# Kernel optimization log

Measured on AMD Instinct MI355X. Metric: run time of the kernel, lower is better.

The kernel has to match this reference:

```python
import jax, jax.numpy as jnp
import numpy as np

N, E, H, L, G = 50000, 500000, 128, 4, 1000
EPS = 1e-7      # GENConv message eps
LN_EPS = 1e-5   # torch LayerNorm default


def setup_inputs() -> dict:
    key = jax.random.key(0)
    ks = jax.random.split(key, 24)
    d = {}
    d["x"] = jax.random.normal(ks[0], (N, 9), jnp.float32)
    d["edge_index"] = jax.random.randint(ks[1], (2, E), 0, N, jnp.int32)
    d["edge_attr"] = jax.random.normal(ks[2], (E, 3), jnp.float32)
    d["batch"] = jnp.sort(jax.random.randint(ks[3], (N,), 0, G, jnp.int32))
    s9, s3, sh, s2h = 1/np.sqrt(9), 1/np.sqrt(3), 1/np.sqrt(H), 1/np.sqrt(2*H)
    u = lambda k, shp, s: jax.random.uniform(k, shp, jnp.float32, -s, s)
    d["enc_node_W"] = u(ks[4], (9, H), s9)
    d["enc_node_b"] = u(ks[5], (H,), s9)
    d["enc_edge_W"] = u(ks[6], (3, H), s3)
    d["enc_edge_b"] = u(ks[7], (H,), s3)
    d["ln_g"] = jnp.ones((L, H), jnp.float32)   # DeepGCNLayer pre-norm affine
    d["ln_b"] = jnp.zeros((L, H), jnp.float32)
    d["W1"] = u(ks[8], (L, H, 2*H), sh)          # GENConv MLP layer 1
    d["b1"] = u(ks[9], (L, 2*H), sh)
    d["mlp_ln_g"] = jnp.ones((L, 2*H), jnp.float32)
    d["mlp_ln_b"] = jnp.zeros((L, 2*H), jnp.float32)
    d["W2"] = u(ks[10], (L, 2*H, H), s2h)        # GENConv MLP layer 2
    d["b2"] = u(ks[11], (L, H), s2h)
    d["t"] = jnp.ones((L,), jnp.float32)         # learnable softmax temperature, init 1.0
    return d


def layernorm(x, g, b):
    mu = x.mean(-1, keepdims=True)
    var = ((x - mu) ** 2).mean(-1, keepdims=True)
    return (x - mu) / jnp.sqrt(var + LN_EPS) * g + b


def genconv(h, src, dst, ea, t, W1, b1, lg, lb, W2, b2):
    # message: relu(x_j + edge_attr) + eps   -> [E, H]
    msg = jax.nn.relu(h[src] + ea) + EPS
    # softmax aggregation over incoming edges, per channel
    logits = t * msg
    m = jax.ops.segment_max(logits, dst, num_segments=N)
    num = jnp.exp(logits - m[dst])
    den = jax.ops.segment_sum(num, dst, num_segments=N)
    alpha = num / den[dst]
    agg = jax.ops.segment_sum(msg * alpha, dst, num_segments=N)
    out = agg + h  # root residual inside GENConv
    z = jax.nn.relu(layernorm(out @ W1 + b1, lg, lb))
    return z @ W2 + b2


def reference(x, edge_index, edge_attr, batch, enc_node_W, enc_node_b,
              enc_edge_W, enc_edge_b, ln_g, ln_b, W1, b1, mlp_ln_g, mlp_ln_b,
              W2, b2, t):
    src, dst = edge_index[0], edge_index[1]
    h = x @ enc_node_W + enc_node_b            # node encoder  [N, H]
    ea = edge_attr @ enc_edge_W + enc_edge_b   # edge encoder  [E, H]
    # layer 0: conv only (DeeperGCN forward uses layers[0].conv directly)
    h = genconv(h, src, dst, ea, t[0], W1[0], b1[0], mlp_ln_g[0], mlp_ln_b[0], W2[0], b2[0])
    # layers 1..L-1: res+ block: x + conv(relu(LN(x))); dropout is identity (eval)
    for i in range(1, L):
        z = jax.nn.relu(layernorm(h, ln_g[i], ln_b[i]))
        h = h + genconv(z, src, dst, ea, t[i], W1[i], b1[i], mlp_ln_g[i], mlp_ln_b[i], W2[i], b2[i])
    h = jax.nn.relu(layernorm(h, ln_g[0], ln_b[0]))  # reuses layer-0 norm
    # global mean pool over graphs
    counts = jax.ops.segment_sum(jnp.ones((N,), h.dtype), batch, num_segments=G)
    sums = jax.ops.segment_sum(h, batch, num_segments=G)
    return sums / jnp.maximum(counts, 1.0)[:, None]
```

## Files before the change

### kernel.cpp

```cpp
#include <hip/hip_runtime.h>

#define NN 50000
#define NE 500000
#define HD 128
#define HD2 256
#define NL 4
#define NG 1000

constexpr float MSG_EPS = 1e-7f;
constexpr float LNEPS   = 1e-5f;

typedef float  f32x4  __attribute__((ext_vector_type(4)));
typedef __bf16 bf16x8 __attribute__((ext_vector_type(8)));

__device__ __forceinline__ unsigned short f2b(float f) {
    unsigned int u = __float_as_uint(f);
    unsigned int r = u + 0x7FFFu + ((u >> 16) & 1u);
    return (unsigned short)(r >> 16);
}
__device__ __forceinline__ float b2f(unsigned short h) {
    return __uint_as_float(((unsigned int)h) << 16);
}

__global__ void k_encode_nodes(const float* __restrict__ x, const float* __restrict__ W,
                               const float* __restrict__ b, unsigned short* __restrict__ zb) {
    int n = blockIdx.x;
    int c = threadIdx.x;
    float xr[9];
#pragma unroll
    for (int k = 0; k < 9; k++) xr[k] = x[n * 9 + k];
    float acc = b[c];
#pragma unroll
    for (int k = 0; k < 9; k++) acc = fmaf(xr[k], W[k * HD + c], acc);
    zb[n * HD + c] = f2b(acc);
}

__global__ void k_prep(const float* __restrict__ W1, const float* __restrict__ W2,
                       unsigned short* __restrict__ W1T, unsigned short* __restrict__ W2T) {
    int idx = blockIdx.x * 256 + threadIdx.x;
    {
        int k = idx & 127, n = (idx >> 7) & 255, l = idx >> 15;
        W1T[idx] = f2b(W1[(l * 128 + k) * 256 + n]);
    }
    {
        int k = idx & 255, n = (idx >> 8) & 127, l = idx >> 15;
        W2T[idx] = f2b(W2[(l * 256 + k) * 128 + n]);
    }
}

__global__ void k_hist(const int* __restrict__ dst, int* __restrict__ counts) {
    int e = blockIdx.x * blockDim.x + threadIdx.x;
    if (e < NE) atomicAdd(&counts[dst[e]], 1);
}

#define SCAN_B 512
__global__ void k_scan1(const int* __restrict__ counts, int* __restrict__ incl,
                        int* __restrict__ bsum) {
    __shared__ int s[SCAN_B];
    int i = blockIdx.x * SCAN_B + threadIdx.x;
    int v = (i < NN) ? counts[i] : 0;
    s[threadIdx.x] = v;
    __syncthreads();
    for (int off = 1; off < SCAN_B; off <<= 1) {
        int t = (threadIdx.x >= off) ? s[threadIdx.x - off] : 0;
        __syncthreads();
        s[threadIdx.x] += t;
        __syncthreads();
    }
    if (i < NN) incl[i] = s[threadIdx.x];
    if (threadIdx.x == SCAN_B - 1) bsum[blockIdx.x] = s[threadIdx.x];
}

__global__ void k_scan2(const int* __restrict__ bsum, int* __restrict__ boff, int nb) {
    __shared__ int s[128];
    int v = (threadIdx.x < nb) ? bsum[threadIdx.x] : 0;
    s[threadIdx.x] = v;
    __syncthreads();
    for (int off = 1; off < 128; off <<= 1) {
        int t = (threadIdx.x >= off) ? s[threadIdx.x - off] : 0;
        __syncthreads();
        s[threadIdx.x] += t;
        __syncthreads();
    }
    if (threadIdx.x < nb) boff[threadIdx.x] = s[threadIdx.x] - v;
}

__global__ void k_scan3(const int* __restrict__ incl, const int* __restrict__ boff,
                        int* __restrict__ row_start) {
    int i = blockIdx.x * SCAN_B + threadIdx.x;
    if (i < NN) row_start[i + 1] = incl[i] + boff[blockIdx.x];
    if (i == 0) row_start[0] = 0;
}

__global__ void k_scatter(const int* __restrict__ src, const int* __restrict__ dst,
                          const float* __restrict__ eattr, const int* __restrict__ row_start,
                          int* __restrict__ cursor, float4* __restrict__ aperm) {
    int e = blockIdx.x * blockDim.x + threadIdx.x;
    if (e >= NE) return;
    int d = dst[e];
    int p = row_start[d] + atomicAdd(&cursor[d], 1);
    float4 v;
    v.x = eattr[e * 3 + 0];
    v.y = eattr[e * 3 + 1];
    v.z = eattr[e * 3 + 2];
    v.w = __int_as_float(src[e]);
    aperm[p] = v;
}

__global__ __launch_bounds__(256) void k_aggregate(const unsigned short* __restrict__ zb,
                                                   const float4* __restrict__ aperm,
                                                   const int* __restrict__ row_start,
                                                   const float* __restrict__ We,
                                                   const float* __restrict__ be,
                                                   const float* __restrict__ t, int layer,
                                                   unsigned int* __restrict__ outb) {
    int w = threadIdx.x >> 6, lane = threadIdx.x & 63;
    int n = blockIdx.x * 4 + w;
    if (n >= NN) return;
    int c = lane * 2;
    float2 w0 = *(const float2*)&We[c];
    float2 w1 = *(const float2*)&We[HD + c];
    float2 w2 = *(const float2*)&We[2 * HD + c];
    float2 bb = *(const float2*)&be[c];
    float tv = t[layer];
    int s0 = row_start[n], s1 = row_start[n + 1];
    float num0 = 0.f, num1 = 0.f, wm0 = 0.f, wm1 = 0.f;
    const unsigned int* z32 = (const unsigned int*)zb;
    int p = s0;
    for (; p + 2 <= s1; p += 2) {
        float4 a0 = aperm[p];
        float4 a1 = aperm[p + 1];
        int sj0 = __float_as_int(a0.w);
        int sj1 = __float_as_int(a1.w);
        unsigned int za = z32[sj0 * 64 + lane];
        unsigned int zc = z32[sj1 * 64 + lane];
        float zax = b2f((unsigned short)za), zay = b2f((unsigned short)(za >> 16));
        float zcx = b2f((unsigned short)zc), zcy = b2f((unsigned short)(zc >> 16));
        float ea0x = fmaf(a0.x, w0.x, fmaf(a0.y, w1.x, fmaf(a0.z, w2.x, bb.x)));
        float ea0y = fmaf(a0.x, w0.y, fmaf(a0.y, w1.y, fmaf(a0.z, w2.y, bb.y)));
        float ea1x = fmaf(a1.x, w0.x, fmaf(a1.y, w1.x, fmaf(a1.z, w2.x, bb.x)));
        float ea1y = fmaf(a1.x, w0.y, fmaf(a1.y, w1.y, fmaf(a1.z, w2.y, bb.y)));
        float m0x = fmaxf(zax + ea0x, 0.f) + MSG_EPS;
        float m0y = fmaxf(zay + ea0y, 0.f) + MSG_EPS;
        float m1x = fmaxf(zcx + ea1x, 0.f) + MSG_EPS;
        float m1y = fmaxf(zcy + ea1y, 0.f) + MSG_EPS;
        float e0x = __expf(tv * m0x), e0y = __expf(tv * m0y);
        float e1x = __expf(tv * m1x), e1y = __expf(tv * m1y);
        num0 += e0x + e1x;
        num1 += e0y + e1y;
        wm0 = fmaf(m0x, e0x, fmaf(m1x, e1x, wm0));
        wm1 = fmaf(m0y, e0y, fmaf(m1y, e1y, wm1));
    }
    if (p < s1) {
        float4 a = aperm[p];
        int sj = __float_as_int(a.w);
        unsigned int za = z32[sj * 64 + lane];
        float zax = b2f((unsigned short)za), zay = b2f((unsigned short)(za >> 16));
        float eax = fmaf(a.x, w0.x, fmaf(a.y, w1.x, fmaf(a.z, w2.x, bb.x)));
        float eay = fmaf(a.x, w0.y, fmaf(a.y, w1.y, fmaf(a.z, w2.y, bb.y)));
        float mx = fmaxf(zax + eax, 0.f) + MSG_EPS;
        float my = fmaxf(zay + eay, 0.f) + MSG_EPS;
        float ex = __expf(tv * mx), ey = __expf(tv * my);
        num0 += ex;
        num1 += ey;
        wm0 = fmaf(mx, ex, wm0);
        wm1 = fmaf(my, ey, wm1);
    }
    unsigned int zn = z32[n * 64 + lane];
    float ox = ((s1 > s0) ? (wm0 / num0) : 0.f) + b2f((unsigned short)zn);
    float oy = ((s1 > s0) ? (wm1 / num1) : 0.f) + b2f((unsigned short)(zn >> 16));
    outb[n * 64 + lane] = (unsigned int)f2b(ox) | ((unsigned int)f2b(oy) << 16);
}

#define HS_LD 268

__global__ __launch_bounds__(64) void k_mlp(const unsigned short* __restrict__ outb,
                                            const unsigned short* __restrict__ W1T,
                                            const float* __restrict__ b1l,
                                            const float* __restrict__ lgl,
                                            const float* __restrict__ lbl,
                                            const unsigned short* __restrict__ W2T,
                                            const float* __restrict__ b2l,
                                            unsigned short* __restrict__ h,
                                            const float* __restrict__ gn,
                                            const float* __restrict__ bn,
                                            unsigned short* __restrict__ zb,
                                            int add_residual) {
    __shared__ __align__(16) unsigned short Hs[16 * HS_LD];

    int base = blockIdx.x * 16;
    int lane = threadIdx.x;
    int q = lane >> 4, i = lane & 15;

    f32x4 acc[16];
#pragma unroll
    for (int ct = 0; ct < 16; ct++) acc[ct] = (f32x4){0.f, 0.f, 0.f, 0.f};

#pragma unroll
    for (int ks = 0; ks < 4; ks++) {
        bf16x8 a = *(const bf16x8*)&outb[(size_t)(base + i) * HD + ks * 32 + q * 8];
#pragma unroll
        for (int ct = 0; ct < 16; ct++) {
            bf16x8 bfr = *(const bf16x8*)&W1T[(ct * 16 + i) * HD + ks * 32 + q * 8];
            acc[ct] = __builtin_amdgcn_mfma_f32_16x16x32_bf16(a, bfr, acc[ct], 0, 0, 0);
        }
    }

#pragma unroll
    for (int ct = 0; ct < 16; ct++) {
        float bb = b1l[ct * 16 + i];
#pragma unroll
        for (int r = 0; r < 4; r++) acc[ct][r] += bb;
    }

    {
        float s[4] = {0.f, 0.f, 0.f, 0.f}, sq[4] = {0.f, 0.f, 0.f, 0.f};
#pragma unroll
        for (int ct = 0; ct < 16; ct++)
#pragma unroll
            for (int r = 0; r < 4; r++) {
                s[r] += acc[ct][r];
                sq[r] = fmaf(acc[ct][r], acc[ct][r], sq[r]);
            }
#pragma unroll
        for (int m = 8; m >= 1; m >>= 1)
#pragma unroll
            for (int r = 0; r < 4; r++) {
                s[r] += __shfl_xor(s[r], m);
                sq[r] += __shfl_xor(sq[r], m);
            }
        float mu[4], inv[4];
#pragma unroll
        for (int r = 0; r < 4; r++) {
            mu[r] = s[r] * (1.f / 256.f);
            float var = sq[r] * (1.f / 256.f) - mu[r] * mu[r];
            inv[r] = rsqrtf(var + LNEPS);
        }
#pragma unroll
        for (int ct = 0; ct < 16; ct++) {
            float g = lgl[ct * 16 + i];
            float c = lbl[ct * 16 + i];
#pragma unroll
            for (int r = 0; r < 4; r++) {
                float v = fmaxf(fmaf((acc[ct][r] - mu[r]) * inv[r], g, c), 0.f);
                Hs[(q * 4 + r) * HS_LD + ct * 16 + i] = f2b(v);
            }
        }
    }

    f32x4 acc2[8];
#pragma unroll
    for (int ct = 0; ct < 8; ct++) acc2[ct] = (f32x4){0.f, 0.f, 0.f, 0.f};

#pragma unroll
    for (int ks = 0; ks < 8; ks++) {
        bf16x8 a = *(const bf16x8*)&Hs[i * HS_LD + ks * 32 + q * 8];
#pragma unroll
        for (int ct = 0; ct < 8; ct++) {
            bf16x8 bfr = *(const bf16x8*)&W2T[(ct * 16 + i) * HD2 + ks * 32 + q * 8];
            acc2[ct] = __builtin_amdgcn_mfma_f32_16x16x32_bf16(a, bfr, acc2[ct], 0, 0, 0);
        }
    }

    if (add_residual) {
#pragma unroll
        for (int ct = 0; ct < 8; ct++) {
            float bb = b2l[ct * 16 + i];
#pragma unroll
            for (int r = 0; r < 4; r++) {
                size_t idx = (size_t)(base + q * 4 + r) * HD + ct * 16 + i;
                acc2[ct][r] += bb + b2f(h[idx]);
            }
        }
    } else {
#pragma unroll
        for (int ct = 0; ct < 8; ct++) {
            float bb = b2l[ct * 16 + i];
#pragma unroll
            for (int r = 0; r < 4; r++) acc2[ct][r] += bb;
        }
    }
#pragma unroll
    for (int ct = 0; ct < 8; ct++)
#pragma unroll
        for (int r = 0; r < 4; r++) {
            size_t idx = (size_t)(base + q * 4 + r) * HD + ct * 16 + i;
            h[idx] = f2b(acc2[ct][r]);
        }

    {
        float s[4] = {0.f, 0.f, 0.f, 0.f}, sq[4] = {0.f, 0.f, 0.f, 0.f};
#pragma unroll
        for (int ct = 0; ct < 8; ct++)
#pragma unroll
            for (int r = 0; r < 4; r++) {
                s[r] += acc2[ct][r];
                sq[r] = fmaf(acc2[ct][r], acc2[ct][r], sq[r]);
            }
#pragma unroll
        for (int m = 8; m >= 1; m >>= 1)
#pragma unroll
            for (int r = 0; r < 4; r++) {
                s[r] += __shfl_xor(s[r], m);
                sq[r] += __shfl_xor(sq[r], m);
            }
        float mu[4], inv[4];
#pragma unroll
        for (int r = 0; r < 4; r++) {
            mu[r] = s[r] * (1.f / 128.f);
            float var = sq[r] * (1.f / 128.f) - mu[r] * mu[r];
            inv[r] = rsqrtf(var + LNEPS);
        }
#pragma unroll
        for (int ct = 0; ct < 8; ct++) {
            float g = gn[ct * 16 + i];
            float c = bn[ct * 16 + i];
#pragma unroll
            for (int r = 0; r < 4; r++) {
                float v = fmaxf(fmaf((acc2[ct][r] - mu[r]) * inv[r], g, c), 0.f);
                zb[(size_t)(base + q * 4 + r) * HD + ct * 16 + i] = f2b(v);
            }
        }
    }
}

__global__ void k_gbounds(const int* __restrict__ batch, int* __restrict__ gstart) {
    int g = blockIdx.x * blockDim.x + threadIdx.x;
    if (g > NG) return;
    int lo = 0, hi = NN;
    while (lo < hi) {
        int mid = (lo + hi) >> 1;
        if (batch[mid] < g) lo = mid + 1;
        else hi = mid;
    }
    gstart[g] = lo;
}

__global__ void k_pool(const unsigned short* __restrict__ zb, const int* __restrict__ gstart,
                       float* __restrict__ out) {
    int g = blockIdx.x;
    int c = threadIdx.x;
    int a = gstart[g], b = gstart[g + 1];
    float s0 = 0.f, s1 = 0.f;
    int n = a;
    for (; n + 2 <= b; n += 2) {
        s0 += b2f(zb[(size_t)n * HD + c]);
        s1 += b2f(zb[(size_t)(n + 1) * HD + c]);
    }
    if (n < b) s0 += b2f(zb[(size_t)n * HD + c]);
    out[g * HD + c] = (s0 + s1) / fmaxf((float)(b - a), 1.f);
}

extern "C" void kernel_launch(void* const* d_in, const int* in_sizes, int n_in, void* d_out,
                              int out_size, void* d_ws, size_t ws_size, hipStream_t stream) {
    const float* x     = (const float*)d_in[0];
    const int* ei      = (const int*)d_in[1];
    const float* eattr = (const float*)d_in[2];
    const int* batch   = (const int*)d_in[3];
    const float* encW  = (const float*)d_in[4];
    const float* encB  = (const float*)d_in[5];
    const float* eW    = (const float*)d_in[6];
    const float* eB    = (const float*)d_in[7];
    const float* ln_g  = (const float*)d_in[8];
    const float* ln_b  = (const float*)d_in[9];
    const float* W1    = (const float*)d_in[10];
    const float* b1    = (const float*)d_in[11];
    const float* mlg   = (const float*)d_in[12];
    const float* mlb   = (const float*)d_in[13];
    const float* W2    = (const float*)d_in[14];
    const float* b2    = (const float*)d_in[15];
    const float* t     = (const float*)d_in[16];
    const int* src = ei;
    const int* dst = ei + NE;

    char* w = (char*)d_ws;
    auto alloc = [&](size_t bytes) {
        char* p = w;
        w += (bytes + 255) & ~size_t(255);
        return p;
    };
    unsigned short* h    = (unsigned short*)alloc(sizeof(unsigned short) * NN * HD);
    unsigned short* zb   = (unsigned short*)alloc(sizeof(unsigned short) * NN * HD);
    unsigned int* outb   = (unsigned int*)alloc(sizeof(unsigned int) * NN * HD / 2);
    float4* aperm        = (float4*)alloc(sizeof(float4) * NE);
    int* row_start       = (int*)alloc(sizeof(int) * (NN + 1));
    int* counts          = (int*)alloc(sizeof(int) * NN);
    int* cursor          = (int*)alloc(sizeof(int) * NN);
    int* incl            = (int*)alloc(sizeof(int) * NN);
    int* bsum            = (int*)alloc(sizeof(int) * 128);
    int* boff            = (int*)alloc(sizeof(int) * 128);
    int* gstart          = (int*)alloc(sizeof(int) * (NG + 1));
    unsigned short* W1T  = (unsigned short*)alloc(sizeof(unsigned short) * NL * HD * HD2);
    unsigned short* W2T  = (unsigned short*)alloc(sizeof(unsigned short) * NL * HD2 * HD);

    hipMemsetAsync(counts, 0, sizeof(int) * NN, stream);
    hipMemsetAsync(cursor, 0, sizeof(int) * NN, stream);

    k_prep<<<512, 256, 0, stream>>>(W1, W2, W1T, W2T);
    k_encode_nodes<<<NN, HD, 0, stream>>>(x, encW, encB, zb);
    k_hist<<<(NE + 255) / 256, 256, 0, stream>>>(dst, counts);
    int nsb = (NN + SCAN_B - 1) / SCAN_B;
    k_scan1<<<nsb, SCAN_B, 0, stream>>>(counts, incl, bsum);
    k_scan2<<<1, 128, 0, stream>>>(bsum, boff, nsb);
    k_scan3<<<nsb, SCAN_B, 0, stream>>>(incl, boff, row_start);
    k_scatter<<<(NE + 255) / 256, 256, 0, stream>>>(src, dst, eattr, row_start, cursor, aperm);
    k_gbounds<<<(NG + 256) / 256, 256, 0, stream>>>(batch, gstart);

    for (int l = 0; l < NL; l++) {
        k_aggregate<<<(NN + 3) / 4, 256, 0, stream>>>(zb, aperm, row_start, eW, eB, t, l, outb);
        int ln_next = (l + 1) % NL;
        k_mlp<<<NN / 16, 64, 0, stream>>>(
            (const unsigned short*)outb, W1T + (size_t)l * HD * HD2, b1 + l * HD2,
            mlg + l * HD2, mlb + l * HD2, W2T + (size_t)l * HD2 * HD, b2 + l * HD, h,
            ln_g + ln_next * HD, ln_b + ln_next * HD, zb, l > 0);
    }
    k_pool<<<NG, HD, 0, stream>>>(zb, gstart, (float*)d_out);
}
```

Measured before the change: 586.1 us.

## Fuse edge aggregation and node MLP into one per-layer kernel

Merges the softmax aggregation kernel and the MFMA MLP kernel into a single kernel per layer. Each wave aggregates 16 nodes into LDS and then feeds that tile straight into the MLP, so the bf16 intermediate buffer never goes through global memory. Ping-pong z buffers are added to avoid read/write hazards across blocks. The edge loop is also unrolled by four to keep more gathers in flight. In exchange, each wave walks its 16 nodes one after another, so parallelism during the aggregation phase drops and per-block LDS use grows, which may reduce occupancy.

```diff
diff --git a/kernel.cpp b/kernel.cpp
--- a/kernel.cpp
+++ b/kernel.cpp
@@ -107,105 +107,91 @@
     aperm[p] = v;
 }
 
-__global__ __launch_bounds__(256) void k_aggregate(const unsigned short* __restrict__ zb,
-                                                   const float4* __restrict__ aperm,
-                                                   const int* __restrict__ row_start,
-                                                   const float* __restrict__ We,
-                                                   const float* __restrict__ be,
-                                                   const float* __restrict__ t, int layer,
-                                                   unsigned int* __restrict__ outb) {
+__device__ __forceinline__ void edge_acc(float4 a, unsigned int zz, float2 w0, float2 w1,
+                                         float2 w2, float2 bb, float tv, float& num0,
+                                         float& num1, float& wm0, float& wm1) {
+    float zx = b2f((unsigned short)zz), zy = b2f((unsigned short)(zz >> 16));
+    float eax = fmaf(a.x, w0.x, fmaf(a.y, w1.x, fmaf(a.z, w2.x, bb.x)));
+    float eay = fmaf(a.x, w0.y, fmaf(a.y, w1.y, fmaf(a.z, w2.y, bb.y)));
+    float mx = fmaxf(zx + eax, 0.f) + MSG_EPS;
+    float my = fmaxf(zy + eay, 0.f) + MSG_EPS;
+    float ex = __expf(tv * mx), ey = __expf(tv * my);
+    num0 += ex;
+    num1 += ey;
+    wm0 = fmaf(mx, ex, wm0);
+    wm1 = fmaf(my, ey, wm1);
+}
+
+#define AS_LD 136
+#define HS_LD 268
+
+__global__ __launch_bounds__(256) void k_layer(
+    const unsigned short* __restrict__ zbin, const float4* __restrict__ aperm,
+    const int* __restrict__ row_start, const float* __restrict__ We,
+    const float* __restrict__ be, const float* __restrict__ t, int layer,
+    const unsigned short* __restrict__ W1T, const float* __restrict__ b1l,
+    const float* __restrict__ lgl, const float* __restrict__ lbl,
+    const unsigned short* __restrict__ W2T, const float* __restrict__ b2l,
+    unsigned short* __restrict__ h, const float* __restrict__ gn,
+    const float* __restrict__ bn, unsigned short* __restrict__ zbout, int add_residual) {
+    __shared__ __align__(16) unsigned short lds[4 * (16 * AS_LD + 16 * HS_LD)];
+
     int w = threadIdx.x >> 6, lane = threadIdx.x & 63;
-    int n = blockIdx.x * 4 + w;
-    if (n >= NN) return;
-    int c = lane * 2;
-    float2 w0 = *(const float2*)&We[c];
-    float2 w1 = *(const float2*)&We[HD + c];
-    float2 w2 = *(const float2*)&We[2 * HD + c];
-    float2 bb = *(const float2*)&be[c];
-    float tv = t[layer];
-    int s0 = row_start[n], s1 = row_start[n + 1];
-    float num0 = 0.f, num1 = 0.f, wm0 = 0.f, wm1 = 0.f;
-    const unsigned int* z32 = (const unsigned int*)zb;
-    int p = s0;
-    for (; p + 2 <= s1; p += 2) {
-        float4 a0 = aperm[p];
-        float4 a1 = aperm[p + 1];
-        int sj0 = __float_as_int(a0.w);
-        int sj1 = __float_as_int(a1.w);
-        unsigned int za = z32[sj0 * 64 + lane];
-        unsigned int zc = z32[sj1 * 64 + lane];
-        float zax = b2f((unsigned short)za), zay = b2f((unsigned short)(za >> 16));
-        float zcx = b2f((unsigned short)zc), zcy = b2f((unsigned short)(zc >> 16));
-        float ea0x = fmaf(a0.x, w0.x, fmaf(a0.y, w1.x, fmaf(a0.z, w2.x, bb.x)));
-        float ea0y = fmaf(a0.x, w0.y, fmaf(a0.y, w1.y, fmaf(a0.z, w2.y, bb.y)));
-        float ea1x = fmaf(a1.x, w0.x, fmaf(a1.y, w1.x, fmaf(a1.z, w2.x, bb.x)));
-        float ea1y = fmaf(a1.x, w0.y, fmaf(a1.y, w1.y, fmaf(a1.z, w2.y, bb.y)));
-        float m0x = fmaxf(zax + ea0x, 0.f) + MSG_EPS;
-        float m0y = fmaxf(zay + ea0y, 0.f) + MSG_EPS;
-        float m1x = fmaxf(zcx + ea1x, 0.f) + MSG_EPS;
-        float m1y = fmaxf(zcy + ea1y, 0.f) + MSG_EPS;
-        float e0x = __expf(tv * m0x), e0y = __expf(tv * m0y);
-        float e1x = __expf(tv * m1x), e1y = __expf(tv * m1y);
-        num0 += e0x + e1x;
-        num1 += e0y + e1y;
-        wm0 = fmaf(m0x, e0x, fmaf(m1x, e1x, wm0));
-        wm1 = fmaf(m0y, e0y, fmaf(m1y, e1y, wm1));
-    }
-    if (p < s1) {
-        float4 a = aperm[p];
-        int sj = __float_as_int(a.w);
-        unsigned int za = z32[sj * 64 + lane];
-        float zax = b2f((unsigned short)za), zay = b2f((unsigned short)(za >> 16));
-        float eax = fmaf(a.x, w0.x, fmaf(a.y, w1.x, fmaf(a.z, w2.x, bb.x)));
-        float eay = fmaf(a.x, w0.y, fmaf(a.y, w1.y, fmaf(a.z, w2.y, bb.y)));
-        float mx = fmaxf(zax + eax, 0.f) + MSG_EPS;
-        float my = fmaxf(zay + eay, 0.f) + MSG_EPS;
-        float ex = __expf(tv * mx), ey = __expf(tv * my);
-        num0 += ex;
-        num1 += ey;
-        wm0 = fmaf(mx, ex, wm0);
-        wm1 = fmaf(my, ey, wm1);
-    }
-    unsigned int zn = z32[n * 64 + lane];
-    float ox = ((s1 > s0) ? (wm0 / num0) : 0.f) + b2f((unsigned short)zn);
-    float oy = ((s1 > s0) ? (wm1 / num1) : 0.f) + b2f((unsigned short)(zn >> 16));
-    outb[n * 64 + lane] = (unsigned int)f2b(ox) | ((unsigned int)f2b(oy) << 16);
-}
-
-#define HS_LD 268
-
-__global__ __launch_bounds__(64) void k_mlp(const unsigned short* __restrict__ outb,
-                                            const unsigned short* __restrict__ W1T,
-                                            const float* __restrict__ b1l,
-                                            const float* __restrict__ lgl,
-                                            const float* __restrict__ lbl,
-                                            const unsigned short* __restrict__ W2T,
-                                            const float* __restrict__ b2l,
-                                            unsigned short* __restrict__ h,
-                                            const float* __restrict__ gn,
-                                            const float* __restrict__ bn,
-                                            unsigned short* __restrict__ zb,
-                                            int add_residual) {
-    __shared__ __align__(16) unsigned short Hs[16 * HS_LD];
-
-    int base = blockIdx.x * 16;
-    int lane = threadIdx.x;
+    int base = blockIdx.x * 64 + w * 16;
+    if (base >= NN) return;
+    unsigned short* As = lds + w * (16 * AS_LD + 16 * HS_LD);
+    unsigned short* Hs = As + 16 * AS_LD;
     int q = lane >> 4, i = lane & 15;
 
+    {
+        int c = lane * 2;
+        float2 w0 = *(const float2*)&We[c];
+        float2 w1 = *(const float2*)&We[HD + c];
+        float2 w2 = *(const float2*)&We[2 * HD + c];
+        float2 bb = *(const float2*)&be[c];
+        float tv = t[layer];
+        const unsigned int* z32 = (const unsigned int*)zbin;
+        unsigned int* As32 = (unsigned int*)As;
+        for (int k = 0; k < 16; k++) {
+            int n = base + k;
+            int s0 = row_start[n], s1 = row_start[n + 1];
+            float num0 = 0.f, num1 = 0.f, wm0 = 0.f, wm1 = 0.f;
+            int p = s0;
+            for (; p + 4 <= s1; p += 4) {
+                float4 a0 = aperm[p], a1 = aperm[p + 1], a2 = aperm[p + 2], a3 = aperm[p + 3];
+                unsigned int zz0 = z32[__float_as_int(a0.w) * 64 + lane];
+                unsigned int zz1 = z32[__float_as_int(a1.w) * 64 + lane];
+                unsigned int zz2 = z32[__float_as_int(a2.w) * 64 + lane];
+                unsigned int zz3 = z32[__float_as_int(a3.w) * 64 + lane];
+                edge_acc(a0, zz0, w0, w1, w2, bb, tv, num0, num1, wm0, wm1);
+                edge_acc(a1, zz1, w0, w1, w2, bb, tv, num0, num1, wm0, wm1);
+                edge_acc(a2, zz2, w0, w1, w2, bb, tv, num0, num1, wm0, wm1);
+                edge_acc(a3, zz3, w0, w1, w2, bb, tv, num0, num1, wm0, wm1);
+            }
+            for (; p < s1; p++) {
+                float4 a = aperm[p];
+                unsigned int zz = z32[__float_as_int(a.w) * 64 + lane];
+                edge_acc(a, zz, w0, w1, w2, bb, tv, num0, num1, wm0, wm1);
+            }
+            unsigned int zn = z32[n * 64 + lane];
+            float ox = ((s1 > s0) ? (wm0 / num0) : 0.f) + b2f((unsigned short)zn);
+            float oy = ((s1 > s0) ? (wm1 / num1) : 0.f) + b2f((unsigned short)(zn >> 16));
+            As32[k * (AS_LD / 2) + lane] = (unsigned int)f2b(ox) | ((unsigned int)f2b(oy) << 16);
+        }
+    }
+
     f32x4 acc[16];
 #pragma unroll
     for (int ct = 0; ct < 16; ct++) acc[ct] = (f32x4){0.f, 0.f, 0.f, 0.f};
-
 #pragma unroll
     for (int ks = 0; ks < 4; ks++) {
-        bf16x8 a = *(const bf16x8*)&outb[(size_t)(base + i) * HD + ks * 32 + q * 8];
+        bf16x8 a = *(const bf16x8*)&As[i * AS_LD + ks * 32 + q * 8];
 #pragma unroll
         for (int ct = 0; ct < 16; ct++) {
             bf16x8 bfr = *(const bf16x8*)&W1T[(ct * 16 + i) * HD + ks * 32 + q * 8];
             acc[ct] = __builtin_amdgcn_mfma_f32_16x16x32_bf16(a, bfr, acc[ct], 0, 0, 0);
         }
     }
-
 #pragma unroll
     for (int ct = 0; ct < 16; ct++) {
         float bb = b1l[ct * 16 + i];
@@ -251,7 +237,6 @@
     f32x4 acc2[8];
 #pragma unroll
     for (int ct = 0; ct < 8; ct++) acc2[ct] = (f32x4){0.f, 0.f, 0.f, 0.f};
-
 #pragma unroll
     for (int ks = 0; ks < 8; ks++) {
         bf16x8 a = *(const bf16x8*)&Hs[i * HS_LD + ks * 32 + q * 8];
@@ -318,7 +303,7 @@
 #pragma unroll
             for (int r = 0; r < 4; r++) {
                 float v = fmaxf(fmaf((acc2[ct][r] - mu[r]) * inv[r], g, c), 0.f);
-                zb[(size_t)(base + q * 4 + r) * HD + ct * 16 + i] = f2b(v);
+                zbout[(size_t)(base + q * 4 + r) * HD + ct * 16 + i] = f2b(v);
             }
         }
     }
@@ -380,8 +365,8 @@
         return p;
     };
     unsigned short* h    = (unsigned short*)alloc(sizeof(unsigned short) * NN * HD);
-    unsigned short* zb   = (unsigned short*)alloc(sizeof(unsigned short) * NN * HD);
-    unsigned int* outb   = (unsigned int*)alloc(sizeof(unsigned int) * NN * HD / 2);
+    unsigned short* zb0  = (unsigned short*)alloc(sizeof(unsigned short) * NN * HD);
+    unsigned short* zb1  = (unsigned short*)alloc(sizeof(unsigned short) * NN * HD);
     float4* aperm        = (float4*)alloc(sizeof(float4) * NE);
     int* row_start       = (int*)alloc(sizeof(int) * (NN + 1));
     int* counts          = (int*)alloc(sizeof(int) * NN);
@@ -397,7 +382,7 @@
     hipMemsetAsync(cursor, 0, sizeof(int) * NN, stream);
 
     k_prep<<<512, 256, 0, stream>>>(W1, W2, W1T, W2T);
-    k_encode_nodes<<<NN, HD, 0, stream>>>(x, encW, encB, zb);
+    k_encode_nodes<<<NN, HD, 0, stream>>>(x, encW, encB, zb0);
     k_hist<<<(NE + 255) / 256, 256, 0, stream>>>(dst, counts);
     int nsb = (NN + SCAN_B - 1) / SCAN_B;
     k_scan1<<<nsb, SCAN_B, 0, stream>>>(counts, incl, bsum);
@@ -406,13 +391,14 @@
     k_scatter<<<(NE + 255) / 256, 256, 0, stream>>>(src, dst, eattr, row_start, cursor, aperm);
     k_gbounds<<<(NG + 256) / 256, 256, 0, stream>>>(batch, gstart);
 
+    int grid = (NN + 63) / 64;
+    unsigned short* zbufs[2] = {zb0, zb1};
     for (int l = 0; l < NL; l++) {
-        k_aggregate<<<(NN + 3) / 4, 256, 0, stream>>>(zb, aperm, row_start, eW, eB, t, l, outb);
         int ln_next = (l + 1) % NL;
-        k_mlp<<<NN / 16, 64, 0, stream>>>(
-            (const unsigned short*)outb, W1T + (size_t)l * HD * HD2, b1 + l * HD2,
-            mlg + l * HD2, mlb + l * HD2, W2T + (size_t)l * HD2 * HD, b2 + l * HD, h,
-            ln_g + ln_next * HD, ln_b + ln_next * HD, zb, l > 0);
-    }
-    k_pool<<<NG, HD, 0, stream>>>(zb, gstart, (float*)d_out);
-}
+        k_layer<<<grid, 256, 0, stream>>>(
+            zbufs[l & 1], aperm, row_start, eW, eB, t, l, W1T + (size_t)l * HD * HD2,
+            b1 + l * HD2, mlg + l * HD2, mlb + l * HD2, W2T + (size_t)l * HD2 * HD, b2 + l * HD,
+            h, ln_g + ln_next * HD, ln_b + ln_next * HD, zbufs[(l + 1) & 1], l > 0);
+    }
+    k_pool<<<NG, HD, 0, stream>>>(zbufs[NL & 1], gstart, (float*)d_out);
+}
```

Result: slower. 815.0 us (+39.1%).
